# Kernel optimization log

Measured on AMD Instinct MI355X. Metric: run time of the kernel, lower is better.

## Reference

```python
import jax, jax.numpy as jnp
import numpy as np

H = 23
Wd = 23
P = H * Wd            # 529 positions per 23x23 score map (hard-coded in the torch module)
B = 16384             # batch of score maps
TH = 0.05             # init kwarg peak_th
KS = 5                # init kwarg ks (max-pool kernel)
BN_EPS = 1e-5


def setup_inputs() -> dict:
    key = jax.random.key(0)
    k = jax.random.split(key, 18)
    def n(i, shape, scale=1.0):
        return scale * jax.random.normal(k[i], shape, dtype=jnp.float32)
    return {
        "target_scores": n(0, (2, B, P)),
        "anno_label": jax.random.uniform(k[1], (1, B, P), dtype=jnp.float32),
        # Conv1d(2->8, k=1) == Linear(2->8); BatchNorm1d in eval mode (running stats)
        "W1": n(2, (8, 2), 0.5), "b1": n(3, (8,), 0.1),
        "g1": 1.0 + n(4, (8,), 0.1), "be1": n(5, (8,), 0.1),
        "m1": n(6, (8,), 0.1), "v1": jax.random.uniform(k[7], (8,), minval=0.5, maxval=1.5),
        "W2": n(8, (8, 8), 0.3), "b2": n(9, (8,), 0.1),
        "g2": 1.0 + n(10, (8,), 0.1), "be2": n(11, (8,), 0.1),
        "m2": n(12, (8,), 0.1), "v2": jax.random.uniform(k[13], (8,), minval=0.5, maxval=1.5),
        "W3": n(14, (1, 8), 0.3), "b3": n(15, (1,), 0.1),
    }


def _find_peaks(scores_flat):
    """find_local_maxima: maxpool(ks, stride 1, pad ks//2) equality + threshold,
    then sort peaks by descending intensity per batch. Fixed-size padded version:
    returns coords [B,P,2] (float), sorted scores [B,P], valid mask [B,P]."""
    s = scores_flat.reshape(-1, H, Wd)
    smax = jax.lax.reduce_window(s, -jnp.inf, jax.lax.max, (1, KS, KS), (1, 1, 1), "SAME")
    mask = ((s == smax) & (s > TH)).reshape(-1, P)
    order = jnp.argsort(-jnp.where(mask, scores_flat, -jnp.inf), axis=1)
    sorted_s = jnp.take_along_axis(scores_flat, order, axis=1)
    valid = jnp.take_along_axis(mask, order, axis=1)
    coords = jnp.stack([(order // Wd).astype(jnp.float32),
                        (order % Wd).astype(jnp.float32)], axis=-1)
    return coords, sorted_s, valid


def _bn(x, g, b, m, v):
    return (x - m) * (g / jnp.sqrt(v + BN_EPS)) + b


def reference(target_scores, anno_label, W1, b1, g1, be1, m1, v1,
              W2, b2, g2, be2, m2, v2, W3, b3):
    scores_old = target_scores[0]            # [B,P]
    scores_cur = target_scores[1]            # [B,P]
    y_old = anno_label[0]                    # [B,P]

    c_old, s_old, val_old = _find_peaks(scores_old)
    c_cur, s_cur, val_cur = _find_peaks(scores_cur)

    # dcf.max2d(train_y_old): argmax coordinate of the training label
    gidx = jnp.argmax(y_old, axis=1)
    gc = jnp.stack([gidx // Wd, gidx % Wd], axis=-1).astype(jnp.float32)   # [B,2]

    # nearest old peak to the ground-truth coordinate
    d2 = jnp.sum((gc[:, None, :] - c_old) ** 2, axis=-1)
    d2 = jnp.where(val_old, d2, jnp.inf)
    pidx = jnp.argmin(d2, axis=1)
    cg = c_old[jnp.arange(c_old.shape[0]), pidx]                           # [B,2]

    # f_old = sum_j s_j * (cg - c_j) over valid old peaks
    sm_old = jnp.where(val_old, s_old, 0.0)
    f_old = jnp.sum(sm_old, axis=1)[:, None] * cg - jnp.einsum("bp,bpd->bd", sm_old, c_old)

    # f_cur[j] = sum_k s_k * (c_j - c_k)  (closed form of the pairwise sum)
    sm_cur = jnp.where(val_cur, s_cur, 0.0)
    S_cur = jnp.sum(sm_cur, axis=1)                                        # [B]
    M_cur = jnp.einsum("bp,bpd->bd", sm_cur, c_cur)                        # [B,2]
    f_cur = S_cur[:, None, None] * c_cur - M_cur[:, None, :]               # [B,P,2]

    diff2 = jnp.sum((f_old[:, None, :] - f_cur) ** 2, axis=-1)
    err = jnp.sqrt(jnp.maximum(diff2, 1e-24))                              # [B,P]

    feats = jnp.stack([err, s_cur], axis=-1)                               # [B,P,2]
    h = jax.nn.relu(_bn(feats @ W1.T + b1, g1, be1, m1, v1))
    h = jax.nn.relu(_bn(h @ W2.T + b2, g2, be2, m2, v2))
    pred = (h @ W3.T + b3)[..., 0]                                         # [B,P]
    pred = jnp.where(val_cur, pred, 0.0)  # only real peaks carry predictions
    return pred, c_cur, s_cur, val_cur
```

## Files before the change

kernel.cpp:

```cpp
#include <hip/hip_runtime.h>
#include <math.h>

#define H_   23
#define W_   23
#define P_   529
#define TH_  0.05f
#define NC   9
#define CAP  96
#define WPB  4
#define NTHR (WPB * 64)
#define WFLO 1154

typedef float f2_t __attribute__((ext_vector_type(2)));

#define WSYNC() do { asm volatile("" ::: "memory"); __builtin_amdgcn_wave_barrier(); } while (0)

__global__ __launch_bounds__(64) void fold_kernel(
    const float* __restrict__ W1, const float* __restrict__ b1,
    const float* __restrict__ g1, const float* __restrict__ be1,
    const float* __restrict__ m1, const float* __restrict__ v1,
    const float* __restrict__ W2, const float* __restrict__ b2,
    const float* __restrict__ g2, const float* __restrict__ be2,
    const float* __restrict__ m2, const float* __restrict__ v2,
    const float* __restrict__ W3, const float* __restrict__ b3,
    float* __restrict__ wf)
{
    const int l = threadIdx.x;
    {
        int o = l >> 3;
        wf[24 + l] = W2[l] * (g2[o] / sqrtf(v2[o] + 1e-5f));
    }
    if (l < 8) {
        float sc1 = g1[l] / sqrtf(v1[l] + 1e-5f);
        wf[2*l]     = W1[2*l] * sc1;
        wf[2*l + 1] = W1[2*l + 1] * sc1;
        wf[16 + l]  = (b1[l] - m1[l]) * sc1 + be1[l];
        float sc2 = g2[l] / sqrtf(v2[l] + 1e-5f);
        wf[88 + l]  = (b2[l] - m2[l]) * sc2 + be2[l];
        wf[96 + l]  = W3[l];
        if (l == 0) wf[104] = b3[0];
    }
}

__global__ __launch_bounds__(NTHR, 8) void peak_kernel(
    const float* __restrict__ tscores,
    const float* __restrict__ anno,
    const float* __restrict__ wf,
    float* __restrict__ out, int B)
{
    const int t  = threadIdx.x;
    const int l  = t & 63;
    const int wv = t >> 6;
    const int b  = blockIdx.x * WPB + wv;
    if (b >= B) return;

    __shared__ float lds[WPB * WFLO];
    float* m  = lds + wv * WFLO;
    float* r  = m + P_;
    float* cs = r;
    int*   cp = (int*)(r + CAP);
    int*   rk = (int*)(r + 2*CAP);
    int*   ri = (int*)r;
    float* ps = r + P_;

    const unsigned long long ltm = (1ull << l) - 1ull;

    const float* yrow = anno + (size_t)b * P_;
    const float* sold = tscores + (size_t)b * P_;
    const float* scur = tscores + (size_t)B * P_ + (size_t)b * P_;
    float ao[NC], so[NC], sc[NC];
    #pragma unroll
    for (int c = 0; c < NC; c++) { int p = 64*c + l; ao[c] = (p < P_) ? yrow[p] : -INFINITY; }
    #pragma unroll
    for (int c = 0; c < NC; c++) { int p = 64*c + l; so[c] = (p < P_) ? sold[p] : 0.f; }
    #pragma unroll
    for (int c = 0; c < NC; c++) { int p = 64*c + l; sc[c] = (p < P_) ? scur[p] : 0.f; }

    float bv = -INFINITY; int bi = 0x7fffffff;
    #pragma unroll
    for (int c = 0; c < NC; c++) {
        int p = 64*c + l;
        if (p < P_ && ao[c] > bv) { bv = ao[c]; bi = p; }
    }
    #pragma unroll
    for (int d = 32; d > 0; d >>= 1) {
        float ov = __shfl_xor(bv, d); int oi = __shfl_xor(bi, d);
        if (ov > bv || (ov == bv && oi < bi)) { bv = ov; bi = oi; }
    }
    const int gy = bi / W_, gx = bi - (bi / W_) * W_;

    auto stage = [&](const float* v) {
        #pragma unroll
        for (int c = 0; c < NC; c++) {
            int p = 64*c + l;
            if (p < P_) m[p] = v[c];
        }
    };
    auto rowmax = [&]() {
        #pragma unroll
        for (int c = 0; c < NC; c++) {
            int p = 64*c + l;
            if (p < P_) {
                int y = p / W_, x = p - (p / W_) * W_;
                const float* row = &m[y * W_];
                float mx = row[x];
                if (x >= 1)      mx = fmaxf(mx, row[x-1]);
                if (x >= 2)      mx = fmaxf(mx, row[x-2]);
                if (x <= W_-2)   mx = fmaxf(mx, row[x+1]);
                if (x <= W_-3)   mx = fmaxf(mx, row[x+2]);
                r[p] = mx;
            }
        }
    };
    auto colmax = [&](int c) {
        int p = 64*c + l;
        int y = p / W_;
        float sm = r[p];
        if (y >= 1)    sm = fmaxf(sm, r[p - W_]);
        if (y >= 2)    sm = fmaxf(sm, r[p - 2*W_]);
        if (y <= H_-2) sm = fmaxf(sm, r[p + W_]);
        if (y <= H_-3) sm = fmaxf(sm, r[p + 2*W_]);
        return sm;
    };

    stage(so);
    WSYNC();
    rowmax();
    WSYNC();
    float So = 0.f, Mor = 0.f, Moc = 0.f;
    float nd2 = INFINITY, ns = -INFINITY; int np = 0;
    #pragma unroll
    for (int c = 0; c < NC; c++) {
        int p = 64*c + l;
        if (p < P_) {
            int y = p / W_, x = p - (p / W_) * W_;
            float s = so[c];
            float sm = colmax(c);
            if (s == sm && s > TH_) {
                So += s; Mor += s * (float)y; Moc += s * (float)x;
                int dy = gy - y, dx = gx - x;
                float d2 = (float)(dy*dy + dx*dx);
                if (d2 < nd2 || (d2 == nd2 && (s > ns || (s == ns && p < np)))) {
                    nd2 = d2; ns = s; np = p;
                }
            }
        }
    }
    #pragma unroll
    for (int d = 32; d > 0; d >>= 1) {
        So += __shfl_xor(So, d); Mor += __shfl_xor(Mor, d); Moc += __shfl_xor(Moc, d);
        float od2 = __shfl_xor(nd2, d), os = __shfl_xor(ns, d); int op = __shfl_xor(np, d);
        if (od2 < nd2 || (od2 == nd2 && (os > ns || (os == ns && op < np)))) {
            nd2 = od2; ns = os; np = op;
        }
    }
    const int cy = np / W_, cx = np - (np / W_) * W_;
    const float foldr = So * (float)cy - Mor;
    const float foldc = So * (float)cx - Moc;

    WSYNC();
    stage(sc);
    WSYNC();
    rowmax();
    WSYNC();
    float Sc = 0.f, Mcr = 0.f, Mcc = 0.f;
    int vb = 0;
    #pragma unroll
    for (int c = 0; c < NC; c++) {
        int p = 64*c + l;
        if (p < P_) {
            int y = p / W_, x = p - (p / W_) * W_;
            float s = sc[c];
            float sm = colmax(c);
            if (s == sm && s > TH_) {
                vb |= 1 << c;
                Sc += s; Mcr += s * (float)y; Mcc += s * (float)x;
            }
        }
    }
    #pragma unroll
    for (int d = 32; d > 0; d >>= 1) {
        Sc += __shfl_xor(Sc, d); Mcr += __shfl_xor(Mcr, d); Mcc += __shfl_xor(Mcc, d);
    }
    WSYNC();

    int K = 0;
    int nb[NC];
    #pragma unroll
    for (int c = 0; c < NC; c++) {
        bool v = (vb >> c) & 1;
        unsigned long long bt = __ballot(v);
        int my = K + __popcll(bt & ltm);
        nb[c] = my;
        if (v && my < CAP) { cs[my] = sc[c]; cp[my] = 64*c + l; }
        K += __popcll(bt);
    }
    WSYNC();

    const int Kc = K > CAP ? CAP : K;
    for (int i = l; i < Kc; i += 64) {
        float si = cs[i]; int pi = cp[i]; int rr = 0;
        for (int j = 0; j < Kc; j++) {
            float sj = cs[j]; int pj = cp[j];
            rr += (sj > si || (sj == si && pj < pi)) ? 1 : 0;
        }
        rk[i] = rr;
    }
    WSYNC();

    auto mlp = [&](int i, float& pv, int& rko) {
        int p = cp[i];
        float s = cs[i];
        rko = rk[i];
        int y = p / W_, x = p - (p / W_) * W_;
        float fcr = Sc * (float)y - Mcr;
        float fcc = Sc * (float)x - Mcc;
        float dr = foldr - fcr, dc = foldc - fcc;
        float err = sqrtf(fmaxf(dr*dr + dc*dc, 1e-24f));
        float h1[8];
        #pragma unroll
        for (int o = 0; o < 8; o++)
            h1[o] = fmaxf(fmaf(err, wf[2*o], fmaf(s, wf[2*o+1], wf[16+o])), 0.f);
        float pred = wf[104];
        #pragma unroll
        for (int o = 0; o < 8; o++) {
            float z = wf[88 + o];
            #pragma unroll
            for (int i2 = 0; i2 < 8; i2++) z = fmaf(h1[i2], wf[24 + o*8 + i2], z);
            pred = fmaf(fmaxf(z, 0.f), wf[96 + o], pred);
        }
        pv = pred;
    };
    float pv0 = 0.f, pv1 = 0.f; int rk0 = -1, rk1 = -1;
    if (l < Kc)      mlp(l, pv0, rk0);
    if (64 + l < Kc) mlp(64 + l, pv1, rk1);
    if (rk0 >= 0) ps[rk0] = pv0;
    if (rk1 >= 0) ps[rk1] = pv1;

    int slot[NC];
    #pragma unroll
    for (int c = 0; c < NC; c++) {
        int p = 64*c + l;
        if (p < P_) {
            bool v = (vb >> c) & 1;
            int n = nb[c];
            slot[c] = v ? ((n < CAP) ? rk[n] : n) : (K + p - n);
        }
    }
    WSYNC();
    #pragma unroll
    for (int c = 0; c < NC; c++) {
        int p = 64*c + l;
        if (p < P_) ri[slot[c]] = p;
    }
    WSYNC();

    const size_t BP = (size_t)B * P_;
    float* out_pred = out;
    float* out_c    = out + BP;
    float* out_s    = out + 3 * BP;
    float* out_v    = out + 4 * BP;
    const size_t rowbase = (size_t)b * P_;

    #pragma unroll
    for (int c = 0; c < NC; c++) {
        int j = 64*c + l;
        if (j < P_) {
            int p = ri[j];
            int y = p / W_, x = p - (p / W_) * W_;
            bool val = j < K;
            float pv = (val && j < CAP) ? ps[j] : 0.f;
            float s  = m[p];
            f2_t co; co.x = (float)y; co.y = (float)x;
            out_pred[rowbase + j] = pv;
            ((f2_t*)out_c)[rowbase + j] = co;
            out_s[rowbase + j] = s;
            out_v[rowbase + j] = val ? 1.f : 0.f;
        }
    }
}

extern "C" void kernel_launch(void* const* d_in, const int* in_sizes, int n_in,
                              void* d_out, int out_size, void* d_ws, size_t ws_size,
                              hipStream_t stream) {
    const int B = in_sizes[0] / (2 * P_);
    float* wf = (float*)d_ws;
    hipLaunchKernelGGL(fold_kernel, dim3(1), dim3(64), 0, stream,
        (const float*)d_in[2], (const float*)d_in[3], (const float*)d_in[4],
        (const float*)d_in[5], (const float*)d_in[6], (const float*)d_in[7],
        (const float*)d_in[8], (const float*)d_in[9], (const float*)d_in[10],
        (const float*)d_in[11], (const float*)d_in[12], (const float*)d_in[13],
        (const float*)d_in[14], (const float*)d_in[15], wf);
    hipLaunchKernelGGL(peak_kernel, dim3((B + WPB - 1) / WPB), dim3(NTHR), 0, stream,
        (const float*)d_in[0], (const float*)d_in[1], (const float*)wf,
        (float*)d_out, B);
}
```

Measured before the change: 81.33 us.

## Fuse weight folding into peak kernel and vectorize LDS reads for rank and MLP

Drops the separate fold kernel: each wave folds BatchNorm into the MLP weights itself and stores them in its own LDS region, so only one launch is needed. The rank-counting loop now reads scores and positions as 4-wide vectors, with the candidate list padded by sentinels to a multiple of four. The MLP reads its folded weights from LDS as float4 rather than scalar global loads. In exchange every wave repeats the tiny fold (extra sqrt and global loads), and the per-wave LDS footprint grows, which may lower occupancy. The early return for b >= B is also removed, so any wave past the batch end would read and write out of range.

After: 96.75 us. +19.0%, slower.

```diff
diff --git a/kernel.cpp b/kernel.cpp
--- a/kernel.cpp
+++ b/kernel.cpp
@@ -9,13 +9,17 @@
 #define CAP  96
 #define WPB  4
 #define NTHR (WPB * 64)
-#define WFLO 1154
+#define WFLO 1272
 
 typedef float f2_t __attribute__((ext_vector_type(2)));
+typedef float f4_t __attribute__((ext_vector_type(4)));
+typedef int   i4_t __attribute__((ext_vector_type(4)));
 
 #define WSYNC() do { asm volatile("" ::: "memory"); __builtin_amdgcn_wave_barrier(); } while (0)
 
-__global__ __launch_bounds__(64) void fold_kernel(
+__global__ __launch_bounds__(NTHR, 8) void peak_kernel(
+    const float* __restrict__ tscores,
+    const float* __restrict__ anno,
     const float* __restrict__ W1, const float* __restrict__ b1,
     const float* __restrict__ g1, const float* __restrict__ be1,
     const float* __restrict__ m1, const float* __restrict__ v1,
@@ -23,47 +27,40 @@
     const float* __restrict__ g2, const float* __restrict__ be2,
     const float* __restrict__ m2, const float* __restrict__ v2,
     const float* __restrict__ W3, const float* __restrict__ b3,
-    float* __restrict__ wf)
-{
-    const int l = threadIdx.x;
-    {
-        int o = l >> 3;
-        wf[24 + l] = W2[l] * (g2[o] / sqrtf(v2[o] + 1e-5f));
-    }
-    if (l < 8) {
-        float sc1 = g1[l] / sqrtf(v1[l] + 1e-5f);
-        wf[2*l]     = W1[2*l] * sc1;
-        wf[2*l + 1] = W1[2*l + 1] * sc1;
-        wf[16 + l]  = (b1[l] - m1[l]) * sc1 + be1[l];
-        float sc2 = g2[l] / sqrtf(v2[l] + 1e-5f);
-        wf[88 + l]  = (b2[l] - m2[l]) * sc2 + be2[l];
-        wf[96 + l]  = W3[l];
-        if (l == 0) wf[104] = b3[0];
-    }
-}
-
-__global__ __launch_bounds__(NTHR, 8) void peak_kernel(
-    const float* __restrict__ tscores,
-    const float* __restrict__ anno,
-    const float* __restrict__ wf,
     float* __restrict__ out, int B)
 {
     const int t  = threadIdx.x;
     const int l  = t & 63;
     const int wv = t >> 6;
     const int b  = blockIdx.x * WPB + wv;
-    if (b >= B) return;
 
     __shared__ float lds[WPB * WFLO];
-    float* m  = lds + wv * WFLO;
-    float* r  = m + P_;
-    float* cs = r;
-    int*   cp = (int*)(r + CAP);
-    int*   rk = (int*)(r + 2*CAP);
-    int*   ri = (int*)r;
-    float* ps = r + P_;
+    float* r   = lds + wv * WFLO;
+    float* m   = r + 532;
+    float* wt  = r + 1064;
+    float* ps  = r + 1176;
+    float* cs  = r;
+    int*   cp  = (int*)(r + 104);
+    int*   rk  = (int*)(r + 208);
+    int*   ri  = (int*)r;
 
     const unsigned long long ltm = (1ull << l) - 1ull;
+
+    {
+        int o = l >> 3;
+        float sc2o = g2[o] / sqrtf(v2[o] + 1e-5f);
+        wt[24 + l] = W2[l] * sc2o;
+        if (l < 8) {
+            float sc1 = g1[l] / sqrtf(v1[l] + 1e-5f);
+            wt[2*l]     = W1[2*l] * sc1;
+            wt[2*l + 1] = W1[2*l + 1] * sc1;
+            wt[16 + l]  = (b1[l] - m1[l]) * sc1 + be1[l];
+            float sc2 = g2[l] / sqrtf(v2[l] + 1e-5f);
+            wt[88 + l]  = (b2[l] - m2[l]) * sc2 + be2[l];
+            wt[96 + l]  = W3[l];
+            if (l == 0) wt[104] = b3[0];
+        }
+    }
 
     const float* yrow = anno + (size_t)b * P_;
     const float* sold = tscores + (size_t)b * P_;
@@ -195,14 +192,21 @@
         if (v && my < CAP) { cs[my] = sc[c]; cp[my] = 64*c + l; }
         K += __popcll(bt);
     }
-    WSYNC();
-
     const int Kc = K > CAP ? CAP : K;
+    if (l == 0) {
+        int e = (Kc + 3) & ~3;
+        for (int j = Kc; j < e; j++) { cs[j] = -INFINITY; cp[j] = 0x7fffffff; }
+    }
+    WSYNC();
+
     for (int i = l; i < Kc; i += 64) {
         float si = cs[i]; int pi = cp[i]; int rr = 0;
-        for (int j = 0; j < Kc; j++) {
-            float sj = cs[j]; int pj = cp[j];
-            rr += (sj > si || (sj == si && pj < pi)) ? 1 : 0;
+        for (int j = 0; j < Kc; j += 4) {
+            f4_t s4 = *(const f4_t*)&cs[j];
+            i4_t p4 = *(const i4_t*)&cp[j];
+            #pragma unroll
+            for (int q = 0; q < 4; q++)
+                rr += (s4[q] > si || (s4[q] == si && p4[q] < pi)) ? 1 : 0;
         }
         rk[i] = rr;
     }
@@ -217,17 +221,31 @@
         float fcc = Sc * (float)x - Mcc;
         float dr = foldr - fcr, dc = foldc - fcc;
         float err = sqrtf(fmaxf(dr*dr + dc*dc, 1e-24f));
+        const f4_t* wq = (const f4_t*)wt;
+        f4_t w1a = wq[0], w1b = wq[1], w1c = wq[2], w1d = wq[3];
+        f4_t b1a = wq[4], b1b = wq[5];
         float h1[8];
-        #pragma unroll
-        for (int o = 0; o < 8; o++)
-            h1[o] = fmaxf(fmaf(err, wf[2*o], fmaf(s, wf[2*o+1], wf[16+o])), 0.f);
-        float pred = wf[104];
+        h1[0] = fmaxf(fmaf(err, w1a[0], fmaf(s, w1a[1], b1a[0])), 0.f);
+        h1[1] = fmaxf(fmaf(err, w1a[2], fmaf(s, w1a[3], b1a[1])), 0.f);
+        h1[2] = fmaxf(fmaf(err, w1b[0], fmaf(s, w1b[1], b1a[2])), 0.f);
+        h1[3] = fmaxf(fmaf(err, w1b[2], fmaf(s, w1b[3], b1a[3])), 0.f);
+        h1[4] = fmaxf(fmaf(err, w1c[0], fmaf(s, w1c[1], b1b[0])), 0.f);
+        h1[5] = fmaxf(fmaf(err, w1c[2], fmaf(s, w1c[3], b1b[1])), 0.f);
+        h1[6] = fmaxf(fmaf(err, w1d[0], fmaf(s, w1d[1], b1b[2])), 0.f);
+        h1[7] = fmaxf(fmaf(err, w1d[2], fmaf(s, w1d[3], b1b[3])), 0.f);
+        f4_t b2a = wq[22], b2b = wq[23];
+        f4_t w3a = wq[24], w3b = wq[25];
+        float pred = wt[104];
         #pragma unroll
         for (int o = 0; o < 8; o++) {
-            float z = wf[88 + o];
-            #pragma unroll
-            for (int i2 = 0; i2 < 8; i2++) z = fmaf(h1[i2], wf[24 + o*8 + i2], z);
-            pred = fmaf(fmaxf(z, 0.f), wf[96 + o], pred);
+            f4_t wa = wq[6 + 2*o], wb = wq[7 + 2*o];
+            float z = (o < 4) ? b2a[o & 3] : b2b[o & 3];
+            z = fmaf(h1[0], wa[0], z); z = fmaf(h1[1], wa[1], z);
+            z = fmaf(h1[2], wa[2], z); z = fmaf(h1[3], wa[3], z);
+            z = fmaf(h1[4], wb[0], z); z = fmaf(h1[5], wb[1], z);
+            z = fmaf(h1[6], wb[2], z); z = fmaf(h1[7], wb[3], z);
+            float w3o = (o < 4) ? w3a[o & 3] : w3b[o & 3];
+            pred = fmaf(fmaxf(z, 0.f), w3o, pred);
         }
         pv = pred;
     };
@@ -284,14 +302,12 @@
                               void* d_out, int out_size, void* d_ws, size_t ws_size,
                               hipStream_t stream) {
     const int B = in_sizes[0] / (2 * P_);
-    float* wf = (float*)d_ws;
-    hipLaunchKernelGGL(fold_kernel, dim3(1), dim3(64), 0, stream,
+    hipLaunchKernelGGL(peak_kernel, dim3((B + WPB - 1) / WPB), dim3(NTHR), 0, stream,
+        (const float*)d_in[0], (const float*)d_in[1],
         (const float*)d_in[2], (const float*)d_in[3], (const float*)d_in[4],
         (const float*)d_in[5], (const float*)d_in[6], (const float*)d_in[7],
         (const float*)d_in[8], (const float*)d_in[9], (const float*)d_in[10],
         (const float*)d_in[11], (const float*)d_in[12], (const float*)d_in[13],
-        (const float*)d_in[14], (const float*)d_in[15], wf);
-    hipLaunchKernelGGL(peak_kernel, dim3((B + WPB - 1) / WPB), dim3(NTHR), 0, stream,
-        (const float*)d_in[0], (const float*)d_in[1], (const float*)wf,
+        (const float*)d_in[14], (const float*)d_in[15],
         (float*)d_out, B);
 }
```
